# Performance work log

Hardware: AMD Instinct MI355X
Metric: run time of the kernel (lower is better)

Reference implementation:

```python
import jax, jax.numpy as jnp
import numpy as np

NEG_W = 0.5  # negative_weight

def setup_inputs() -> dict:
    key = jax.random.key(0)
    ks = jax.random.split(key, 11)
    U, V, P, F, D, NF = 16384, 50000, 65536, 20, 64, 100000
    return {
        "user_emb": jax.random.normal(ks[0], (NF, D), jnp.float32),
        "item_emb": jax.random.normal(ks[1], (NF, D), jnp.float32),
        "w_user": jax.random.normal(ks[2], (NF,), jnp.float32),
        "w_item": jax.random.normal(ks[3], (NF,), jnp.float32),
        "bias": jax.random.normal(ks[4], (1,), jnp.float32),
        "h1": jax.random.normal(ks[5], (D,), jnp.float32),
        "h2": jax.random.normal(ks[6], (D,), jnp.float32),
        "user_feat_idx": jax.random.randint(ks[7], (U, F), 0, NF, jnp.int32),
        "item_feat_idx": jax.random.randint(ks[8], (V, F), 0, NF, jnp.int32),
        "pos_user_ids": jax.random.randint(ks[9], (P,), 0, U, jnp.int32),
        "pos_item_ids": jax.random.randint(ks[10], (P,), 0, V, jnp.int32),
    }

def _entity_terms(emb, w, feat_idx, h1, extra):
    # emb: [NF,D], feat_idx: [N,F] -> batched gather + FM bi-interaction
    g = emb[feat_idx]                      # [N,F,D]
    s = g.sum(axis=1)                      # [N,D]  (p_ud / q_vd)
    bi = 0.5 * (jnp.square(s) - jnp.square(g).sum(axis=1))  # [N,D]
    scalar = bi @ h1 + w[feat_idx].sum(axis=1) + extra       # [N]
    return s, scalar

def reference(user_emb, item_emb, w_user, w_item, bias, h1, h2,
              user_feat_idx, item_feat_idx, pos_user_ids, pos_item_ids):
    U = user_feat_idx.shape[0]
    V = item_feat_idx.shape[0]
    ones_u = jnp.ones((U, 1), user_emb.dtype)
    ones_v = jnp.ones((V, 1), item_emb.dtype)

    p_ud, su = _entity_terms(user_emb, w_user, user_feat_idx, h1, bias[0])
    q_vd, sv = _entity_terms(item_emb, w_item, item_feat_idx, h1, 0.0)
    p_u = jnp.concatenate([p_ud, su[:, None], ones_u], axis=1)  # [U,D+2]
    q_v = jnp.concatenate([q_vd, ones_v, sv[:, None]], axis=1)  # [V,D+2]

    # negative (all-pairs) term via D x D Gram matrices
    A = p_ud.T @ p_ud                                           # [D,D]
    B = q_vd.T @ q_vd                                           # [D,D]
    loss_neg = NEG_W * jnp.einsum('i,j,ij,ij->', h2, h2, A, B)

    # positive-pair term
    hv = jnp.concatenate([h2, jnp.ones((2,), h2.dtype)])        # [D+2]
    y = jnp.einsum('pd,pd,d->p', p_u[pos_user_ids], q_v[pos_item_ids], hv)
    loss_pos = jnp.sum((1.0 - NEG_W) * jnp.square(y) - 2.0 * y)

    return jnp.reshape(loss_neg + loss_pos, (1,))
```

## Files before the change

kernel.cpp:

```cpp
#include <hip/hip_runtime.h>

#define FD 20
#define DD 64

#define GA 64
#define GB 128
#define POSB 2048
#define NEGB 64

typedef float float4v __attribute__((ext_vector_type(4)));
typedef unsigned short ushort4v __attribute__((ext_vector_type(4)));
typedef unsigned short ushort8v __attribute__((ext_vector_type(8)));

__device__ __forceinline__ unsigned short f2bf(float f) {
    unsigned u = __float_as_uint(f);
    unsigned r = u + 0x7fffu + ((u >> 16) & 1u);
    return (unsigned short)(r >> 16);
}
__device__ __forceinline__ float bf2f(unsigned short h) {
    return __uint_as_float((unsigned)h << 16);
}

__global__ __launch_bounds__(256) void conv_kernel(
    const float* __restrict__ ue, const float* __restrict__ ie,
    unsigned int* __restrict__ u8, unsigned int* __restrict__ i8,
    int n4, float* __restrict__ out, int out_size)
{
    int i = blockIdx.x * blockDim.x + threadIdx.x;
    if (i < out_size) out[i] = 0.0f;
    if (i >= 2 * n4) return;
    const float4v* src; unsigned int* dst; int k;
    if (i < n4) { src = (const float4v*)ue; dst = u8; k = i; }
    else        { src = (const float4v*)ie; dst = i8; k = i - n4; }
    float4v v = src[k];
    unsigned int p = 0;
    p = __builtin_amdgcn_cvt_pk_fp8_f32(v.x, v.y, p, false);
    p = __builtin_amdgcn_cvt_pk_fp8_f32(v.z, v.w, p, true);
    dst[k] = p;
}

__global__ __launch_bounds__(256, 4) void entity_kernel(
    const unsigned char* __restrict__ user_f8,
    const unsigned char* __restrict__ item_f8,
    const float* __restrict__ w_user, const float* __restrict__ w_item,
    const float* __restrict__ bias, const float* __restrict__ h1,
    const int* __restrict__ ufeat, const int* __restrict__ ifeat,
    unsigned short* __restrict__ p_bf, float* __restrict__ su,
    unsigned short* __restrict__ q_bf, float* __restrict__ sv,
    int U, int V)
{
    int wid  = (int)((blockIdx.x * blockDim.x + threadIdx.x) >> 6);
    int lane = threadIdx.x & 63;
    if (wid >= U + V) return;

    const unsigned char* emb; const float* wv; const int* fidx; float extra;
    unsigned short* srow; float* sc;
    if (wid < U) {
        emb = user_f8; wv = w_user; fidx = ufeat + (size_t)wid * FD;
        extra = bias[0]; srow = p_bf + (size_t)wid * DD; sc = su + wid;
    } else {
        int m = wid - U;
        emb = item_f8; wv = w_item; fidx = ifeat + (size_t)m * FD;
        extra = 0.0f; srow = q_bf + (size_t)m * DD; sc = sv + m;
    }

    int myidx = 0; float myw = 0.0f;
    if (lane < FD) {
        myidx = fidx[lane];
        myw   = wv[myidx];
    }

    int grp = lane >> 4;
    int c   = lane & 15;

    int fx[5];
#pragma unroll
    for (int i = 0; i < 5; ++i)
        fx[i] = __shfl(myidx, grp + 4 * i, 64);

    unsigned int hw[5];
#pragma unroll
    for (int i = 0; i < 5; ++i)
        hw[i] = *((const unsigned int*)(emb + (size_t)fx[i] * DD) + c);

    float4v s4 = (float4v)0.0f, ss4 = (float4v)0.0f;
#pragma unroll
    for (int i = 0; i < 5; ++i) {
        float4v g;
        g.x = __builtin_amdgcn_cvt_f32_fp8(hw[i], 0);
        g.y = __builtin_amdgcn_cvt_f32_fp8(hw[i], 1);
        g.z = __builtin_amdgcn_cvt_f32_fp8(hw[i], 2);
        g.w = __builtin_amdgcn_cvt_f32_fp8(hw[i], 3);
        s4 += g; ss4 += g * g;
    }

#pragma unroll
    for (int off = 16; off <= 32; off <<= 1) {
        float4v t, u;
        t.x = __shfl_xor(s4.x,  off, 64); t.y = __shfl_xor(s4.y,  off, 64);
        t.z = __shfl_xor(s4.z,  off, 64); t.w = __shfl_xor(s4.w,  off, 64);
        u.x = __shfl_xor(ss4.x, off, 64); u.y = __shfl_xor(ss4.y, off, 64);
        u.z = __shfl_xor(ss4.z, off, 64); u.w = __shfl_xor(ss4.w, off, 64);
        s4 += t; ss4 += u;
    }

    float part = myw;
    if (grp == 0) {
        float4v h14 = *(const float4v*)(h1 + c * 4);
        float4v bi4 = 0.5f * (s4 * s4 - ss4);
        part += bi4.x*h14.x + bi4.y*h14.y + bi4.z*h14.z + bi4.w*h14.w;
        ushort4v o;
        o.x = f2bf(s4.x); o.y = f2bf(s4.y); o.z = f2bf(s4.z); o.w = f2bf(s4.w);
        *(ushort4v*)(srow + c * 4) = o;
    }

#pragma unroll
    for (int off = 1; off <= 32; off <<= 1)
        part += __shfl_xor(part, off, 64);

    if (lane == 0) *sc = part + extra;
}

__device__ __forceinline__ void gram_block(
    const unsigned short* __restrict__ M, int nrows, int bid, int nblk,
    float* __restrict__ Gpart)
{
    __shared__ float tile[64][64];
    int t  = threadIdx.x;
    int i0 = (t & 15) << 2;
    int j0 = (t >> 4) << 2;
    float acc[4][4] = {};

    int ntiles = (nrows + 63) >> 6;
    for (int tt = bid; tt < ntiles; tt += nblk) {
        int row0 = tt << 6;
        __syncthreads();
#pragma unroll
        for (int k = 0; k < 2; ++k) {
            int fi = t + k * 256;
            int r  = fi >> 3;
            int c8 = (fi & 7) << 3;
            ushort8v hv = (ushort8v)0;
            if (row0 + r < nrows)
                hv = *(const ushort8v*)(M + (size_t)(row0 + r) * DD + c8);
            float4v lo, hi;
            lo.x = bf2f(hv[0]); lo.y = bf2f(hv[1]);
            lo.z = bf2f(hv[2]); lo.w = bf2f(hv[3]);
            hi.x = bf2f(hv[4]); hi.y = bf2f(hv[5]);
            hi.z = bf2f(hv[6]); hi.w = bf2f(hv[7]);
            *(float4v*)&tile[r][c8]     = lo;
            *(float4v*)&tile[r][c8 + 4] = hi;
        }
        __syncthreads();
        for (int n = 0; n < 64; ++n) {
            float4v va = *(const float4v*)&tile[n][i0];
            float4v vb = *(const float4v*)&tile[n][j0];
#pragma unroll
            for (int a = 0; a < 4; ++a)
#pragma unroll
                for (int b = 0; b < 4; ++b)
                    acc[a][b] += va[a] * vb[b];
        }
    }
    float* out = Gpart + (size_t)bid * (DD * DD);
#pragma unroll
    for (int a = 0; a < 4; ++a)
#pragma unroll
        for (int b = 0; b < 4; ++b)
            out[(i0 + a) * DD + (j0 + b)] = acc[a][b];
}

__global__ __launch_bounds__(256) void mid_kernel(
    const unsigned short* __restrict__ p_bf, int U, float* __restrict__ PA,
    const unsigned short* __restrict__ q_bf, int V, float* __restrict__ PB,
    const float* __restrict__ su, const float* __restrict__ sv,
    const float* __restrict__ h2,
    const int* __restrict__ pu, const int* __restrict__ pi,
    int P, float* __restrict__ posPart)
{
    if (blockIdx.x < GA) { gram_block(p_bf, U, blockIdx.x, GA, PA); return; }
    if (blockIdx.x < GA + GB) { gram_block(q_bf, V, blockIdx.x - GA, GB, PB); return; }

    __shared__ float red[4];
    int lane = threadIdx.x & 63;
    int sl   = lane & 15;
    int sub  = lane >> 4;
    int pb   = blockIdx.x - (GA + GB);
    int wId  = pb * 4 + (threadIdx.x >> 6);
    const int NW = POSB * 4;

    float4v h2v = *(const float4v*)(h2 + sl * 4);

    int pid0 = wId * 4 + sub;
    int pid1 = pid0 + NW * 4;
    bool ok0 = pid0 < P, ok1 = pid1 < P;

    int u0 = 0, v0 = 0, u1 = 0, v1 = 0;
    if (ok0) { u0 = pu[pid0]; v0 = pi[pid0]; }
    if (ok1) { u1 = pu[pid1]; v1 = pi[pid1]; }

    ushort4v ph0 = (ushort4v)0, qh0 = (ushort4v)0;
    ushort4v ph1 = (ushort4v)0, qh1 = (ushort4v)0;
    if (ok0) {
        ph0 = *(const ushort4v*)(p_bf + (size_t)u0 * DD + sl * 4);
        qh0 = *(const ushort4v*)(q_bf + (size_t)v0 * DD + sl * 4);
    }
    if (ok1) {
        ph1 = *(const ushort4v*)(p_bf + (size_t)u1 * DD + sl * 4);
        qh1 = *(const ushort4v*)(q_bf + (size_t)v1 * DD + sl * 4);
    }

    float d0 = bf2f(ph0.x)*bf2f(qh0.x)*h2v.x + bf2f(ph0.y)*bf2f(qh0.y)*h2v.y
             + bf2f(ph0.z)*bf2f(qh0.z)*h2v.z + bf2f(ph0.w)*bf2f(qh0.w)*h2v.w;
    float d1 = bf2f(ph1.x)*bf2f(qh1.x)*h2v.x + bf2f(ph1.y)*bf2f(qh1.y)*h2v.y
             + bf2f(ph1.z)*bf2f(qh1.z)*h2v.z + bf2f(ph1.w)*bf2f(qh1.w)*h2v.w;
#pragma unroll
    for (int off = 1; off < 16; off <<= 1) {
        d0 += __shfl_xor(d0, off, 64);
        d1 += __shfl_xor(d1, off, 64);
    }

    float acc = 0.0f;
    if (sl == 0) {
        if (ok0) { float y = d0 + su[u0] + sv[v0]; acc += 0.5f * y * y - 2.0f * y; }
        if (ok1) { float y = d1 + su[u1] + sv[v1]; acc += 0.5f * y * y - 2.0f * y; }
    }
    acc += __shfl_xor(acc, 16, 64);
    acc += __shfl_xor(acc, 32, 64);
    if (lane == 0) red[threadIdx.x >> 6] = acc;
    __syncthreads();
    if (threadIdx.x == 0)
        posPart[pb] = red[0] + red[1] + red[2] + red[3];
}

__global__ __launch_bounds__(256) void neg_reduce_kernel(
    const float* __restrict__ PA, const float* __restrict__ PB,
    const float* __restrict__ h2, const float* __restrict__ posPart,
    float* __restrict__ out)
{
    __shared__ float sA[4][64], sB[4][64];
    __shared__ float sPos;
    int t  = threadIdx.x;
    int l  = t & 63;
    int ch = t >> 6;
    int e  = blockIdx.x * 64 + l;

    float a = 0.0f, b = 0.0f;
#pragma unroll
    for (int k = 0; k < GA / 4; ++k)
        a += PA[(size_t)(ch * (GA / 4) + k) * (DD * DD) + e];
#pragma unroll
    for (int k = 0; k < GB / 4; ++k)
        b += PB[(size_t)(ch * (GB / 4) + k) * (DD * DD) + e];
    sA[ch][l] = a;
    sB[ch][l] = b;

    if (ch == 1) {
        float p = (l < POSB / NEGB) ? posPart[blockIdx.x * (POSB / NEGB) + l] : 0.0f;
#pragma unroll
        for (int off = 1; off <= 32; off <<= 1)
            p += __shfl_xor(p, off, 64);
        if (l == 0) sPos = p;
    }
    __syncthreads();

    if (ch == 0) {
        float fa = sA[0][l] + sA[1][l] + sA[2][l] + sA[3][l];
        float fb = sB[0][l] + sB[1][l] + sB[2][l] + sB[3][l];
        float acc = 0.5f * h2[blockIdx.x] * h2[l] * fa * fb;
#pragma unroll
        for (int off = 1; off <= 32; off <<= 1)
            acc += __shfl_xor(acc, off, 64);
        if (l == 0)
            atomicAdd(out, acc + sPos);
    }
}

extern "C" void kernel_launch(void* const* d_in, const int* in_sizes, int n_in,
                              void* d_out, int out_size, void* d_ws, size_t ws_size,
                              hipStream_t stream)
{
    const float* user_emb = (const float*)d_in[0];
    const float* item_emb = (const float*)d_in[1];
    const float* w_user   = (const float*)d_in[2];
    const float* w_item   = (const float*)d_in[3];
    const float* bias     = (const float*)d_in[4];
    const float* h1       = (const float*)d_in[5];
    const float* h2       = (const float*)d_in[6];
    const int*   ufeat    = (const int*)d_in[7];
    const int*   ifeat    = (const int*)d_in[8];
    const int*   pu       = (const int*)d_in[9];
    const int*   pi       = (const int*)d_in[10];

    const int NF = in_sizes[0] / DD;
    const int U  = in_sizes[7] / FD;
    const int V  = in_sizes[8] / FD;
    const int P  = in_sizes[9];

    float* ws = (float*)d_ws;
    size_t off = 0;
    unsigned short* p_bf = (unsigned short*)(ws + off); off += (size_t)U * DD / 2;
    unsigned short* q_bf = (unsigned short*)(ws + off); off += (size_t)V * DD / 2;
    float* su   = ws + off; off += (size_t)U;          off = (off + 63) & ~(size_t)63;
    float* sv   = ws + off; off += (size_t)V;          off = (off + 63) & ~(size_t)63;
    float* PA   = ws + off; off += (size_t)GA * DD * DD;
    float* PB   = ws + off; off += (size_t)GB * DD * DD;
    float* posPart = ws + off; off += (size_t)POSB;    off = (off + 63) & ~(size_t)63;
    unsigned char* uf8 = (unsigned char*)(ws + off);   off += (size_t)NF * DD / 4;
    unsigned char* if8 = (unsigned char*)(ws + off);   off += (size_t)NF * DD / 4;

    float* out = (float*)d_out;

    int n4 = NF * DD / 4;
    conv_kernel<<<(2 * n4 + 255) / 256, 256, 0, stream>>>(
        user_emb, item_emb, (unsigned int*)uf8, (unsigned int*)if8,
        n4, out, out_size);

    int nent = U + V;
    entity_kernel<<<(nent + 3) / 4, 256, 0, stream>>>(
        uf8, if8, w_user, w_item, bias, h1,
        ufeat, ifeat, p_bf, su, q_bf, sv, U, V);

    mid_kernel<<<GA + GB + POSB, 256, 0, stream>>>(
        p_bf, U, PA, q_bf, V, PB, su, sv, h2, pu, pi, P, posPart);

    neg_reduce_kernel<<<NEGB, 256, 0, stream>>>(PA, PB, h2, posPart, out);
}
```

Measured before the change: 154.3 us.

## Compute Gram matrices with bf16 MFMA per wave, exploiting symmetry

Replaces the scalar FP32 outer-product Gram accumulation with per-wave bf16 MFMA 16x16x32 instructions. Each wave stages 64-row tiles in XOR-swizzled LDS and computes only the 10 upper-triangular 16x16 blocks. The reduction kernel reads the mirrored index for lower-triangular entries. Gram work is packed into four waves per block, which frees block slots for the positive-pair work but leaves per-element strided LDS reads for the fragments.

```diff
diff --git a/kernel.cpp b/kernel.cpp
--- a/kernel.cpp
+++ b/kernel.cpp
@@ -5,12 +5,15 @@
 
 #define GA 64
 #define GB 128
+#define GAB 16
+#define GBB 32
 #define POSB 2048
 #define NEGB 64
 
 typedef float float4v __attribute__((ext_vector_type(4)));
 typedef unsigned short ushort4v __attribute__((ext_vector_type(4)));
 typedef unsigned short ushort8v __attribute__((ext_vector_type(8)));
+typedef short short8v __attribute__((ext_vector_type(8)));
 
 __device__ __forceinline__ unsigned short f2bf(float f) {
     unsigned u = __float_as_uint(f);
@@ -121,53 +124,63 @@
     if (lane == 0) *sc = part + extra;
 }
 
-__device__ __forceinline__ void gram_block(
-    const unsigned short* __restrict__ M, int nrows, int bid, int nblk,
-    float* __restrict__ Gpart)
-{
-    __shared__ float tile[64][64];
-    int t  = threadIdx.x;
-    int i0 = (t & 15) << 2;
-    int j0 = (t >> 4) << 2;
-    float acc[4][4] = {};
+__device__ __forceinline__ void gram_block_mfma(
+    const unsigned short* __restrict__ M, int nrows, int gwid, int nw,
+    float* __restrict__ Gpart, unsigned short* __restrict__ sm)
+{
+    int lane = threadIdx.x & 63;
+    int q = lane >> 4;
+    int c = lane & 15;
+
+    float4v acc[10];
+#pragma unroll
+    for (int t = 0; t < 10; ++t) acc[t] = (float4v)0.0f;
 
     int ntiles = (nrows + 63) >> 6;
-    for (int tt = bid; tt < ntiles; tt += nblk) {
+    for (int tt = gwid; tt < ntiles; tt += nw) {
         int row0 = tt << 6;
-        __syncthreads();
-#pragma unroll
-        for (int k = 0; k < 2; ++k) {
-            int fi = t + k * 256;
-            int r  = fi >> 3;
-            int c8 = (fi & 7) << 3;
+#pragma unroll
+        for (int p = 0; p < 8; ++p) {
+            int r  = p * 8 + (lane >> 3);
+            int ch = lane & 7;
             ushort8v hv = (ushort8v)0;
             if (row0 + r < nrows)
-                hv = *(const ushort8v*)(M + (size_t)(row0 + r) * DD + c8);
-            float4v lo, hi;
-            lo.x = bf2f(hv[0]); lo.y = bf2f(hv[1]);
-            lo.z = bf2f(hv[2]); lo.w = bf2f(hv[3]);
-            hi.x = bf2f(hv[4]); hi.y = bf2f(hv[5]);
-            hi.z = bf2f(hv[6]); hi.w = bf2f(hv[7]);
-            *(float4v*)&tile[r][c8]     = lo;
-            *(float4v*)&tile[r][c8 + 4] = hi;
+                hv = *(const ushort8v*)(M + (size_t)(row0 + r) * DD + ch * 8);
+            int X = (p & 3) << 1;
+            *(ushort8v*)(sm + r * 64 + ((ch ^ X) << 3)) = hv;
         }
-        __syncthreads();
-        for (int n = 0; n < 64; ++n) {
-            float4v va = *(const float4v*)&tile[n][i0];
-            float4v vb = *(const float4v*)&tile[n][j0];
-#pragma unroll
-            for (int a = 0; a < 4; ++a)
-#pragma unroll
-                for (int b = 0; b < 4; ++b)
-                    acc[a][b] += va[a] * vb[b];
+#pragma unroll
+        for (int kb2 = 0; kb2 < 2; ++kb2) {
+            int k0 = kb2 * 32 + q * 8;
+            int X  = q << 1;
+            const unsigned short* rb = sm + k0 * 64 + (c & 7);
+            short8v f[4];
+#pragma unroll
+            for (int Db = 0; Db < 4; ++Db) {
+                int chunk = (Db * 2 + (c >> 3)) ^ X;
+                const unsigned short* b = rb + chunk * 8;
+                short8v fv;
+#pragma unroll
+                for (int j = 0; j < 8; ++j)
+                    fv[j] = (short)b[j * 64];
+                f[Db] = fv;
+            }
+#define MM(i_, j_, t_) acc[t_] = __builtin_amdgcn_mfma_f32_16x16x32_bf16(f[i_], f[j_], acc[t_], 0, 0, 0);
+            MM(0,0,0) MM(0,1,1) MM(0,2,2) MM(0,3,3) MM(1,1,4)
+            MM(1,2,5) MM(1,3,6) MM(2,2,7) MM(2,3,8) MM(3,3,9)
+#undef MM
         }
     }
-    float* out = Gpart + (size_t)bid * (DD * DD);
-#pragma unroll
-    for (int a = 0; a < 4; ++a)
-#pragma unroll
-        for (int b = 0; b < 4; ++b)
-            out[(i0 + a) * DD + (j0 + b)] = acc[a][b];
+
+    float* out = Gpart + (size_t)gwid * (DD * DD);
+#define ST(i_, j_, t_)                                                     \
+    {                                                                      \
+        for (int rg = 0; rg < 4; ++rg)                                     \
+            out[(i_ * 16 + q * 4 + rg) * DD + j_ * 16 + c] = acc[t_][rg];  \
+    }
+    ST(0,0,0) ST(0,1,1) ST(0,2,2) ST(0,3,3) ST(1,1,4)
+    ST(1,2,5) ST(1,3,6) ST(2,2,7) ST(2,3,8) ST(3,3,9)
+#undef ST
 }
 
 __global__ __launch_bounds__(256) void mid_kernel(
@@ -178,14 +191,23 @@
     const int* __restrict__ pu, const int* __restrict__ pi,
     int P, float* __restrict__ posPart)
 {
-    if (blockIdx.x < GA) { gram_block(p_bf, U, blockIdx.x, GA, PA); return; }
-    if (blockIdx.x < GA + GB) { gram_block(q_bf, V, blockIdx.x - GA, GB, PB); return; }
-
+    __shared__ unsigned short gtiles[4][64 * 64];
     __shared__ float red[4];
+    int w = threadIdx.x >> 6;
+
+    if (blockIdx.x < GAB) {
+        gram_block_mfma(p_bf, U, blockIdx.x * 4 + w, GA, PA, gtiles[w]);
+        return;
+    }
+    if (blockIdx.x < GAB + GBB) {
+        gram_block_mfma(q_bf, V, (blockIdx.x - GAB) * 4 + w, GB, PB, gtiles[w]);
+        return;
+    }
+
     int lane = threadIdx.x & 63;
     int sl   = lane & 15;
     int sub  = lane >> 4;
-    int pb   = blockIdx.x - (GA + GB);
+    int pb   = blockIdx.x - (GAB + GBB);
     int wId  = pb * 4 + (threadIdx.x >> 6);
     const int NW = POSB * 4;
 
@@ -243,7 +265,8 @@
     int t  = threadIdx.x;
     int l  = t & 63;
     int ch = t >> 6;
-    int e  = blockIdx.x * 64 + l;
+    int i  = blockIdx.x;
+    int e  = ((i >> 4) <= (l >> 4)) ? (i * 64 + l) : (l * 64 + i);
 
     float a = 0.0f, b = 0.0f;
 #pragma unroll
@@ -321,7 +344,7 @@
         uf8, if8, w_user, w_item, bias, h1,
         ufeat, ifeat, p_bf, su, q_bf, sv, U, V);
 
-    mid_kernel<<<GA + GB + POSB, 256, 0, stream>>>(
+    mid_kernel<<<GAB + GBB + POSB, 256, 0, stream>>>(
         p_bf, U, PA, q_bf, V, PB, su, sv, h2, pu, pi, P, posPart);
 
     neg_reduce_kernel<<<NEGB, 256, 0, stream>>>(PA, PB, h2, posPart, out);
```

After: 168.0 us. 8.9% more time.
